# Kernel optimization log

Measured on AMD Instinct MI355X. Metric: run time of the kernel, lower is better.

## Reference

```python
import jax, jax.numpy as jnp
import numpy as np

N_NODES = 100000
N_EDGES = 1600000
D_IN = 128
D_OUT = 128


def setup_inputs() -> dict:
    key = jax.random.key(0)
    k1, k2, k3, k4, k5 = jax.random.split(key, 5)
    features = jax.random.normal(k1, (N_NODES, D_IN), dtype=jnp.float32)
    edge_row = jax.random.randint(k2, (N_EDGES,), 0, N_NODES, dtype=jnp.int32)
    edge_col = jax.random.randint(k3, (N_EDGES,), 0, N_NODES, dtype=jnp.int32)
    edge_val = jax.random.uniform(k4, (N_EDGES,), dtype=jnp.float32)
    # Xavier-uniform weight, zero bias, ones skip weight (matches reset_parameters)
    limit = float(np.sqrt(6.0 / (D_IN + D_OUT)))
    weight = jax.random.uniform(k5, (D_IN, D_OUT), minval=-limit, maxval=limit, dtype=jnp.float32)
    bias = jnp.zeros((D_OUT,), dtype=jnp.float32)
    skip_weight = jnp.ones((D_OUT,), dtype=jnp.float32)
    return {"features": features, "edge_row": edge_row, "edge_col": edge_col,
            "edge_val": edge_val, "weight": weight, "bias": bias,
            "skip_weight": skip_weight}


def reference(features, edge_row, edge_col, edge_val, weight, bias, skip_weight):
    # Dense projection: [N, Din] @ [Din, Dout] -> [N, Dout]
    h = features @ weight
    # SpMM in COO form: Ah[r] = sum_e val[e] * h[col[e]] for edges with row[e]==r
    gathered = edge_val[:, None] * h[edge_col]          # [E, Dout]
    Ah = jax.ops.segment_sum(gathered, edge_row, num_segments=N_NODES)
    # Skip-scale + bias + activation epilogue
    out = h * skip_weight[None, :] + Ah + bias[None, :]
    return jax.nn.selu(out)
```

## Files before the change

### kernel.cpp

```cpp
#include <hip/hip_runtime.h>

#define N_NODES 100000
#define N_EDGES 1600000
#define D 128
#define BM 64
#define GEMM_BLKS 1563

#define BROWS 128
#define NB 782
#define EB 250
#define EPB 6400
#define NTAB (NB * EB)
#define SCAN_BLKS 191

#define SPMM_BLKS 6250

typedef __attribute__((ext_vector_type(8))) short short8_t;
typedef __attribute__((ext_vector_type(4))) float float4_t;
typedef __attribute__((ext_vector_type(2))) float f32x2_t;

__device__ __forceinline__ unsigned pack_bf16x2(float a, float b) {
    unsigned ua = __float_as_uint(a);
    unsigned ub = __float_as_uint(b);
    ua = (ua + 0x7fffu + ((ua >> 16) & 1u)) >> 16;
    ub = (ub + 0x7fffu + ((ub >> 16) & 1u)) & 0xffff0000u;
    return ua | ub;
}

__device__ __forceinline__ float selu_f(float x) {
    const float SCALE = 1.0507009873554805f;
    const float ALPHA = 1.6732632423543772f;
    return x > 0.f ? SCALE * x : SCALE * ALPHA * (expf(x) - 1.f);
}

__global__ __launch_bounds__(256) void bhist_prep_kernel(
    const int* __restrict__ erow, const float* __restrict__ W,
    unsigned* __restrict__ tbl, unsigned short* __restrict__ wt)
{
    __shared__ unsigned hcnt[NB];
    const int t = threadIdx.x;
    if (blockIdx.x < EB) {
        const int k = blockIdx.x;
        for (int i = t; i < NB; i += 256) hcnt[i] = 0;
        __syncthreads();
        const int4* q = (const int4*)(erow + k * EPB);
        for (int i = t; i < EPB / 4; i += 256) {
            const int4 r = q[i];
            atomicAdd(&hcnt[r.x >> 7], 1u);
            atomicAdd(&hcnt[r.y >> 7], 1u);
            atomicAdd(&hcnt[r.z >> 7], 1u);
            atomicAdd(&hcnt[r.w >> 7], 1u);
        }
        __syncthreads();
        for (int i = t; i < NB; i += 256) tbl[k * NB + i] = hcnt[i];
    } else {
        const int pb = blockIdx.x - EB;
        for (int idx = pb * 4096 + t; idx < (pb + 1) * 4096; idx += 256) {
            const int k = idx >> 7, n = idx & 127;
            unsigned u = __float_as_uint(W[idx]);
            u = (u + 0x7fffu + ((u >> 16) & 1u)) >> 16;
            wt[n * D + k] = (unsigned short)u;
        }
    }
}

__global__ __launch_bounds__(1024) void scan_local_kernel(
    const unsigned* __restrict__ tbl, unsigned* __restrict__ lex,
    unsigned* __restrict__ bsum)
{
    __shared__ unsigned wsum[16];
    const int t = threadIdx.x;
    const int L = blockIdx.x * 1024 + t;
    const int lane = t & 63;

    unsigned v = 0;
    if (L < NTAB) {
        const int b = L / EB;
        const int k = L - b * EB;
        v = tbl[k * NB + b];
    }
    unsigned x = v;
#pragma unroll
    for (int d = 1; d < 64; d <<= 1) {
        const unsigned y = __shfl_up(x, d, 64);
        if (lane >= d) x += y;
    }
    if (lane == 63) wsum[t >> 6] = x;
    __syncthreads();
    unsigned add = 0;
    for (int w = 0; w < (t >> 6); ++w) add += wsum[w];
    x += add;
    if (L < NTAB) lex[L] = x - v;
    if (t == 1023) bsum[blockIdx.x] = x;
}

__global__ __launch_bounds__(256) void bscatter_kernel(
    const int* __restrict__ erow, const int* __restrict__ ecol,
    const float* __restrict__ eval_, const unsigned* __restrict__ lex,
    const unsigned* __restrict__ bsum, unsigned* __restrict__ tbl,
    int2* __restrict__ rec)
{
    __shared__ unsigned bp[192];
    __shared__ unsigned wtot[4];
    __shared__ unsigned base[NB], rk[NB];
    const int t = threadIdx.x;
    const int k = blockIdx.x;

    unsigned v = 0, x = 0;
    if (t < 192) {
        v = (t < SCAN_BLKS) ? bsum[t] : 0u;
        x = v;
#pragma unroll
        for (int d = 1; d < 64; d <<= 1) {
            const unsigned y = __shfl_up(x, d, 64);
            if ((t & 63) >= d) x += y;
        }
        if ((t & 63) == 63) wtot[t >> 6] = x;
    }
    __syncthreads();
    if (t < 192) {
        unsigned add = 0;
        if (t >= 64)  add += wtot[0];
        if (t >= 128) add += wtot[1];
        bp[t] = x - v + add;
    }
    __syncthreads();

    for (int b = t; b < NB; b += 256) {
        const int L = b * EB + k;
        const unsigned bs_ = lex[L] + bp[L >> 10];
        base[b] = bs_;
        rk[b] = 0;
        if (k == 0) tbl[b] = bs_;
    }
    __syncthreads();

    const int4*   qr = (const int4*)(erow + k * EPB);
    const int4*   qc = (const int4*)(ecol + k * EPB);
    const float4* qv = (const float4*)(eval_ + k * EPB);

    for (int i = t; i < EPB / 4; i += 256) {
        const int4   r = qr[i];
        const int4   c = qc[i];
        const float4 vv = qv[i];
        {
            const int b = r.x >> 7;
            const unsigned pos = base[b] + atomicAdd(&rk[b], 1u);
            rec[pos] = make_int2(c.x | ((r.x & 127) << 17), __float_as_int(vv.x));
        }
        {
            const int b = r.y >> 7;
            const unsigned pos = base[b] + atomicAdd(&rk[b], 1u);
            rec[pos] = make_int2(c.y | ((r.y & 127) << 17), __float_as_int(vv.y));
        }
        {
            const int b = r.z >> 7;
            const unsigned pos = base[b] + atomicAdd(&rk[b], 1u);
            rec[pos] = make_int2(c.z | ((r.z & 127) << 17), __float_as_int(vv.z));
        }
        {
            const int b = r.w >> 7;
            const unsigned pos = base[b] + atomicAdd(&rk[b], 1u);
            rec[pos] = make_int2(c.w | ((r.w & 127) << 17), __float_as_int(vv.w));
        }
    }
}

__global__ __launch_bounds__(256) void gemm_bsort_kernel(
    const float* __restrict__ feat, const unsigned short* __restrict__ wt,
    unsigned* __restrict__ h16,
    const unsigned* __restrict__ tbl, const int2* __restrict__ rec,
    int2* __restrict__ rec2, unsigned* __restrict__ rstart)
{
    __shared__ __align__(16) char smem[52224];
    const int t = threadIdx.x;

    if (blockIdx.x < GEMM_BLKS) {
        short* At = (short*)smem;
        short* Wt = (short*)(smem + 17408);
        const int rowBase = blockIdx.x * BM;

        {
            const int n = t >> 1, hf = t & 1;
            const uint4* src = (const uint4*)(wt + n * D + hf * 64);
            uint4* dst = (uint4*)&Wt[n * 136 + hf * 64];
#pragma unroll
            for (int j = 0; j < 8; ++j) dst[j] = src[j];
        }
        {
#pragma unroll
            for (int i = 0; i < 8; ++i) {
                const int p = t + 256 * i;
                const int r = p >> 5, kq = p & 31;
                int row = rowBase + r;
                if (row >= N_NODES) row = N_NODES - 1;
                const float4 f = *(const float4*)&feat[(size_t)row * D + kq * 4];
                uint2 u;
                u.x = pack_bf16x2(f.x, f.y);
                u.y = pack_bf16x2(f.z, f.w);
                *(uint2*)&At[r * 136 + kq * 4] = u;
            }
        }
        __syncthreads();

        const int w = t >> 6, lane = t & 63;
        const int m16 = lane & 15, kg = lane >> 4;

        short8_t a_frag[4];
        const int arow = w * 16 + m16;
#pragma unroll
        for (int k0 = 0; k0 < 4; ++k0)
            a_frag[k0] = *(const short8_t*)&At[arow * 136 + k0 * 32 + kg * 8];

#pragma unroll
        for (int nt = 0; nt < 8; ++nt) {
            float4_t acc = {0.f, 0.f, 0.f, 0.f};
#pragma unroll
            for (int k0 = 0; k0 < 4; ++k0) {
                const short8_t b =
                    *(const short8_t*)&Wt[(nt * 16 + m16) * 136 + k0 * 32 + kg * 8];
                acc = __builtin_amdgcn_mfma_f32_16x16x32_bf16(a_frag[k0], b, acc, 0, 0, 0);
            }
            float mine[4], part[4];
#pragma unroll
            for (int i = 0; i < 4; ++i) {
                mine[i] = acc[i];
                part[i] = __shfl_xor(mine[i], 1, 64);
            }
            if ((m16 & 1) == 0) {
                const int cp = (nt * 16 + m16) >> 1;
#pragma unroll
                for (int i = 0; i < 4; ++i) {
                    const int row = rowBase + w * 16 + kg * 4 + i;
                    if (row < N_NODES)
                        h16[(size_t)row * 64 + cp] = pack_bf16x2(mine[i], part[i]);
                }
            }
        }
    } else {
        unsigned* cnt  = (unsigned*)smem;
        unsigned* bas  = cnt + BROWS;
        unsigned* rk   = bas + BROWS;
        unsigned* w0p  = rk + BROWS;
        const int b = blockIdx.x - GEMM_BLKS;

        if (t < BROWS) { cnt[t] = 0; rk[t] = 0; }
        __syncthreads();

        const unsigned s = tbl[b];
        const unsigned e = (b == NB - 1) ? (unsigned)N_EDGES : tbl[b + 1];

        for (unsigned j = s + t; j < e; j += 256)
            atomicAdd(&cnt[(rec[j].x >> 17) & 127], 1u);
        __syncthreads();

        unsigned v = 0, x = 0;
        if (t < BROWS) {
            v = cnt[t]; x = v;
#pragma unroll
            for (int d = 1; d < 64; d <<= 1) {
                const unsigned y = __shfl_up(x, d, 64);
                if ((t & 63) >= d) x += y;
            }
        }
        if (t == 63) w0p[0] = x;
        __syncthreads();
        if (t < BROWS) {
            const unsigned ex = x - v + ((t >= 64) ? w0p[0] : 0u);
            bas[t] = s + ex;
            const int row = b * BROWS + t;
            if (row < N_NODES) rstart[row] = s + ex;
        }
        __syncthreads();

        for (unsigned j = s + t; j < e; j += 256) {
            const int2 R = rec[j];
            const int rl = (R.x >> 17) & 127;
            const unsigned pos = bas[rl] + atomicAdd(&rk[rl], 1u);
            rec2[pos] = R;
        }
    }
}

__global__ __launch_bounds__(256) void spmm_csr_kernel(
    const unsigned* __restrict__ rstart, const int2* __restrict__ rec,
    const unsigned* __restrict__ h16, const float* __restrict__ skip,
    const float* __restrict__ bias, float* __restrict__ out)
{
    const int lane = threadIdx.x & 63;
    const int wid  = threadIdx.x >> 6;
    const int rowBase = (blockIdx.x * 4 + wid) * 4;

    const int c2 = lane * 2;
    const float2 sk = *(const float2*)&skip[c2];
    const float2 bs = *(const float2*)&bias[c2];

    unsigned sb[5];
#pragma unroll
    for (int i = 0; i < 5; ++i) {
        const int rr = rowBase + i;
        const unsigned bnd = (rr < N_NODES) ? rstart[rr] : (unsigned)N_EDGES;
        sb[i] = (unsigned)__builtin_amdgcn_readfirstlane((int)bnd);
    }

#pragma unroll
    for (int r = 0; r < 4; ++r) {
        const int row = rowBase + r;
        const unsigned s = sb[r];
        const unsigned e = sb[r + 1];
        const unsigned n = e - s;
        const unsigned nfull = n >> 3;

        float ax = 0.f, ay = 0.f, bx = 0.f, by = 0.f;

        int2 E0[8], E1[8];
        unsigned g0[8], g1[8];

        auto LOADREC = [&](int2 (&E)[8], unsigned base) {
#pragma unroll
            for (int k = 0; k < 8; ++k) E[k] = rec[base + k];
        };
        auto GATHER = [&](unsigned (&g)[8], const int2 (&E)[8]) {
#pragma unroll
            for (int k = 0; k < 8; ++k)
                g[k] = h16[(size_t)(((unsigned)E[k].x) & 0x1FFFFu) * 64 + lane];
        };
        auto FMA8 = [&](const int2 (&E)[8], const unsigned (&g)[8]) {
#pragma unroll
            for (int k = 0; k < 8; ++k) {
                const float v = __int_as_float(E[k].y);
                if (k & 1) {
                    bx = fmaf(v, __uint_as_float(g[k] << 16), bx);
                    by = fmaf(v, __uint_as_float(g[k] & 0xffff0000u), by);
                } else {
                    ax = fmaf(v, __uint_as_float(g[k] << 16), ax);
                    ay = fmaf(v, __uint_as_float(g[k] & 0xffff0000u), ay);
                }
            }
        };

        if (nfull) {
            LOADREC(E0, s);
            GATHER(g0, E0);
            unsigned bi = 1;
            for (; bi + 1 < nfull; bi += 2) {
                LOADREC(E1, s + bi * 8);
                GATHER(g1, E1);
                FMA8(E0, g0);
                LOADREC(E0, s + (bi + 1) * 8);
                GATHER(g0, E0);
                FMA8(E1, g1);
            }
            if (bi < nfull) {
                LOADREC(E1, s + bi * 8);
                GATHER(g1, E1);
                FMA8(E0, g0);
                FMA8(E1, g1);
            } else {
                FMA8(E0, g0);
            }
        }

        const unsigned tn = n & 7;
        if (tn) {
            const unsigned tb = s + nfull * 8;
            int2 Et[8];
            unsigned gt[8];
#pragma unroll
            for (int k = 0; k < 8; ++k) {
                const unsigned idx = tb + (unsigned)k;
                Et[k] = rec[idx < e ? idx : e - 1u];
            }
#pragma unroll
            for (int k = 0; k < 8; ++k)
                gt[k] = h16[(size_t)(((unsigned)Et[k].x) & 0x1FFFFu) * 64 + lane];
#pragma unroll
            for (int k = 0; k < 8; ++k) {
                const float v = (tb + (unsigned)k < e) ? __int_as_float(Et[k].y) : 0.f;
                if (k & 1) {
                    bx = fmaf(v, __uint_as_float(gt[k] << 16), bx);
                    by = fmaf(v, __uint_as_float(gt[k] & 0xffff0000u), by);
                } else {
                    ax = fmaf(v, __uint_as_float(gt[k] << 16), ax);
                    ay = fmaf(v, __uint_as_float(gt[k] & 0xffff0000u), ay);
                }
            }
        }

        const unsigned hw = h16[(size_t)row * 64 + lane];
        float ox = fmaf(__uint_as_float(hw << 16),         sk.x, (ax + bx) + bs.x);
        float oy = fmaf(__uint_as_float(hw & 0xffff0000u), sk.y, (ay + by) + bs.y);
        ox = selu_f(ox);
        oy = selu_f(oy);
        f32x2_t o;
        o.x = ox;
        o.y = oy;
        __builtin_nontemporal_store(o, (f32x2_t*)&out[(size_t)row * D + c2]);
    }
}

__global__ __launch_bounds__(256) void gemm_fb_kernel(
    const float* __restrict__ feat, const float* __restrict__ W,
    const float* __restrict__ bias, const float* __restrict__ skip,
    float* __restrict__ h, float* __restrict__ out)
{
    __shared__ float Wl[D * D];
    __shared__ float Fl[32 * D];
    const int tid = threadIdx.x;

    const float4* W4 = (const float4*)W;
    float4* Wl4 = (float4*)Wl;
#pragma unroll
    for (int i = 0; i < 16; ++i) Wl4[tid + 256 * i] = W4[tid + 256 * i];

    const size_t rowBase = (size_t)blockIdx.x * 32;
    const float4* F4 = (const float4*)(feat + rowBase * D);
    float4* Fl4 = (float4*)Fl;
#pragma unroll
    for (int i = 0; i < 4; ++i) Fl4[tid + 256 * i] = F4[tid + 256 * i];
    __syncthreads();

    const int colg = (tid & 31) * 4;
    const int row0 = (tid >> 5) * 4;
    float4 acc[4];
#pragma unroll
    for (int r = 0; r < 4; ++r) acc[r] = make_float4(0.f, 0.f, 0.f, 0.f);
#pragma unroll 4
    for (int k = 0; k < D; ++k) {
        const float4 w = *(const float4*)&Wl[k * D + colg];
#pragma unroll
        for (int r = 0; r < 4; ++r) {
            const float aa = Fl[(row0 + r) * D + k];
            acc[r].x += aa * w.x; acc[r].y += aa * w.y;
            acc[r].z += aa * w.z; acc[r].w += aa * w.w;
        }
    }
    const float4 sk = *(const float4*)&skip[colg];
    const float4 bs = *(const float4*)&bias[colg];
#pragma unroll
    for (int r = 0; r < 4; ++r) {
        const size_t row = rowBase + row0 + r;
        *(float4*)&h[row * D + colg] = acc[r];
        float4 o;
        o.x = acc[r].x * sk.x + bs.x; o.y = acc[r].y * sk.y + bs.y;
        o.z = acc[r].z * sk.z + bs.z; o.w = acc[r].w * sk.w + bs.w;
        *(float4*)&out[row * D + colg] = o;
    }
}

__global__ __launch_bounds__(256) void spmm_atomic_kernel(
    const int* __restrict__ erow, const int* __restrict__ ecol,
    const float* __restrict__ eval_, const float* __restrict__ h,
    float* __restrict__ out)
{
    const int e = blockIdx.x * 4 + (threadIdx.x >> 6);
    if (e >= N_EDGES) return;
    const int lane = threadIdx.x & 63;
    const int r = erow[e];
    const int c = ecol[e];
    const float v = eval_[e];
    const float2 hv = *(const float2*)&h[(size_t)c * D + lane * 2];
    float* o = &out[(size_t)r * D + lane * 2];
    atomicAdd(o + 0, v * hv.x);
    atomicAdd(o + 1, v * hv.y);
}

__global__ __launch_bounds__(256) void selu_kernel(float* __restrict__ out)
{
    const size_t i = (size_t)blockIdx.x * blockDim.x + threadIdx.x;
    float4 v = ((float4*)out)[i];
    v.x = selu_f(v.x); v.y = selu_f(v.y); v.z = selu_f(v.z); v.w = selu_f(v.w);
    ((float4*)out)[i] = v;
}

extern "C" void kernel_launch(void* const* d_in, const int* in_sizes, int n_in,
                              void* d_out, int out_size, void* d_ws, size_t ws_size,
                              hipStream_t stream)
{
    const float* feat  = (const float*)d_in[0];
    const int*   erow  = (const int*)d_in[1];
    const int*   ecol  = (const int*)d_in[2];
    const float* eval_ = (const float*)d_in[3];
    const float* W     = (const float*)d_in[4];
    const float* bias  = (const float*)d_in[5];
    const float* skip  = (const float*)d_in[6];

    float* out = (float*)d_out;

    const size_t off_h16  = 0;
    const size_t off_tbl  = 25600000;
    const size_t off_lex  = 26382000;
    const size_t off_bs   = 27164336;
    const size_t off_rst  = 27165360;
    const size_t off_wt   = 27565360;
    const size_t off_rec  = 27598128;
    const size_t off_rec2 = 40398128;
    const size_t needed   = 53198128;

    char* ws = (char*)d_ws;
    unsigned*       h16    = (unsigned*)(ws + off_h16);
    unsigned*       tbl    = (unsigned*)(ws + off_tbl);
    unsigned*       lex    = (unsigned*)(ws + off_lex);
    unsigned*       bsum   = (unsigned*)(ws + off_bs);
    unsigned*       rstart = (unsigned*)(ws + off_rst);
    unsigned short* wt     = (unsigned short*)(ws + off_wt);
    int2*           rec    = (int2*)(ws + off_rec);
    int2*           rec2   = (int2*)(ws + off_rec2);

    if (ws_size >= needed) {
        bhist_prep_kernel<<<EB + 4, 256, 0, stream>>>(erow, W, tbl, wt);
        scan_local_kernel<<<SCAN_BLKS, 1024, 0, stream>>>(tbl, lex, bsum);
        bscatter_kernel<<<EB, 256, 0, stream>>>(erow, ecol, eval_, lex, bsum, tbl, rec);
        gemm_bsort_kernel<<<GEMM_BLKS + NB, 256, 0, stream>>>(
            feat, wt, h16, tbl, rec, rec2, rstart);
        spmm_csr_kernel<<<SPMM_BLKS, 256, 0, stream>>>(
            rstart, rec2, h16, skip, bias, out);
    } else {
        float* h = (float*)d_ws;
        gemm_fb_kernel<<<N_NODES / 32, 256, 0, stream>>>(feat, W, bias, skip, h, out);
        spmm_atomic_kernel<<<N_EDGES / 4, 256, 0, stream>>>(erow, ecol, eval_, h, out);
        selu_kernel<<<(N_NODES * D) / (256 * 4), 256, 0, stream>>>(out);
    }
}
```

Baseline: 125.5 us.

## Split SpMM feature columns across blocks and edges across lane groups

After: 187.4 us. 1.49x slower.

```diff
diff --git a/kernel.cpp b/kernel.cpp
--- a/kernel.cpp
+++ b/kernel.cpp
@@ -13,7 +13,7 @@
 #define NTAB (NB * EB)
 #define SCAN_BLKS 191
 
-#define SPMM_BLKS 6250
+#define SPMM_BLKS 25000
 
 typedef __attribute__((ext_vector_type(8))) short short8_t;
 typedef __attribute__((ext_vector_type(4))) float float4_t;
@@ -289,11 +289,15 @@
 {
     const int lane = threadIdx.x & 63;
     const int wid  = threadIdx.x >> 6;
-    const int rowBase = (blockIdx.x * 4 + wid) * 4;
-
-    const int c2 = lane * 2;
-    const float2 sk = *(const float2*)&skip[c2];
-    const float2 bs = *(const float2*)&bias[c2];
+    const int q    = blockIdx.x & 3;
+    const int rowBase = ((blockIdx.x >> 2) * 4 + wid) * 4;
+
+    const int el  = lane >> 4;
+    const int dwq = (lane & 15) + q * 16;
+    const int c0  = dwq * 2;
+
+    const float skx = skip[c0], sky = skip[c0 + 1];
+    const float bsx = bias[c0], bsy = bias[c0 + 1];
 
     unsigned sb[5];
 #pragma unroll
@@ -308,94 +312,44 @@
         const int row = rowBase + r;
         const unsigned s = sb[r];
         const unsigned e = sb[r + 1];
-        const unsigned n = e - s;
-        const unsigned nfull = n >> 3;
-
-        float ax = 0.f, ay = 0.f, bx = 0.f, by = 0.f;
-
-        int2 E0[8], E1[8];
-        unsigned g0[8], g1[8];
-
-        auto LOADREC = [&](int2 (&E)[8], unsigned base) {
-#pragma unroll
-            for (int k = 0; k < 8; ++k) E[k] = rec[base + k];
-        };
-        auto GATHER = [&](unsigned (&g)[8], const int2 (&E)[8]) {
-#pragma unroll
-            for (int k = 0; k < 8; ++k)
-                g[k] = h16[(size_t)(((unsigned)E[k].x) & 0x1FFFFu) * 64 + lane];
-        };
-        auto FMA8 = [&](const int2 (&E)[8], const unsigned (&g)[8]) {
-#pragma unroll
-            for (int k = 0; k < 8; ++k) {
-                const float v = __int_as_float(E[k].y);
-                if (k & 1) {
-                    bx = fmaf(v, __uint_as_float(g[k] << 16), bx);
-                    by = fmaf(v, __uint_as_float(g[k] & 0xffff0000u), by);
-                } else {
-                    ax = fmaf(v, __uint_as_float(g[k] << 16), ax);
-                    ay = fmaf(v, __uint_as_float(g[k] & 0xffff0000u), ay);
-                }
-            }
-        };
-
-        if (nfull) {
-            LOADREC(E0, s);
-            GATHER(g0, E0);
-            unsigned bi = 1;
-            for (; bi + 1 < nfull; bi += 2) {
-                LOADREC(E1, s + bi * 8);
-                GATHER(g1, E1);
-                FMA8(E0, g0);
-                LOADREC(E0, s + (bi + 1) * 8);
-                GATHER(g0, E0);
-                FMA8(E1, g1);
-            }
-            if (bi < nfull) {
-                LOADREC(E1, s + bi * 8);
-                GATHER(g1, E1);
-                FMA8(E0, g0);
-                FMA8(E1, g1);
-            } else {
-                FMA8(E0, g0);
-            }
-        }
-
-        const unsigned tn = n & 7;
-        if (tn) {
-            const unsigned tb = s + nfull * 8;
-            int2 Et[8];
-            unsigned gt[8];
-#pragma unroll
-            for (int k = 0; k < 8; ++k) {
-                const unsigned idx = tb + (unsigned)k;
-                Et[k] = rec[idx < e ? idx : e - 1u];
-            }
-#pragma unroll
-            for (int k = 0; k < 8; ++k)
-                gt[k] = h16[(size_t)(((unsigned)Et[k].x) & 0x1FFFFu) * 64 + lane];
-#pragma unroll
-            for (int k = 0; k < 8; ++k) {
-                const float v = (tb + (unsigned)k < e) ? __int_as_float(Et[k].y) : 0.f;
-                if (k & 1) {
-                    bx = fmaf(v, __uint_as_float(gt[k] << 16), bx);
-                    by = fmaf(v, __uint_as_float(gt[k] & 0xffff0000u), by);
-                } else {
-                    ax = fmaf(v, __uint_as_float(gt[k] << 16), ax);
-                    ay = fmaf(v, __uint_as_float(gt[k] & 0xffff0000u), ay);
-                }
-            }
-        }
-
-        const unsigned hw = h16[(size_t)row * 64 + lane];
-        float ox = fmaf(__uint_as_float(hw << 16),         sk.x, (ax + bx) + bs.x);
-        float oy = fmaf(__uint_as_float(hw & 0xffff0000u), sk.y, (ay + by) + bs.y);
-        ox = selu_f(ox);
-        oy = selu_f(oy);
-        f32x2_t o;
-        o.x = ox;
-        o.y = oy;
-        __builtin_nontemporal_store(o, (f32x2_t*)&out[(size_t)row * D + c2]);
+
+        float ax = 0.f, ay = 0.f;
+
+        for (unsigned j = s; j < e; j += 16) {
+            int2     E[4];
+            unsigned g[4];
+            float    v[4];
+#pragma unroll
+            for (int k = 0; k < 4; ++k) {
+                const unsigned idx = j + (unsigned)(el + 4 * k);
+                const unsigned ji  = idx < e ? idx : e - 1u;
+                E[k] = rec[ji];
+                v[k] = (idx < e) ? __int_as_float(E[k].y) : 0.f;
+            }
+#pragma unroll
+            for (int k = 0; k < 4; ++k)
+                g[k] = h16[(size_t)(((unsigned)E[k].x) & 0x1FFFFu) * 64 + dwq];
+#pragma unroll
+            for (int k = 0; k < 4; ++k) {
+                ax = fmaf(v[k], __uint_as_float(g[k] << 16), ax);
+                ay = fmaf(v[k], __uint_as_float(g[k] & 0xffff0000u), ay);
+            }
+        }
+
+        ax += __shfl_xor(ax, 16, 64);
+        ax += __shfl_xor(ax, 32, 64);
+        ay += __shfl_xor(ay, 16, 64);
+        ay += __shfl_xor(ay, 32, 64);
+
+        if (el == 0) {
+            const unsigned hw = h16[(size_t)row * 64 + dwq];
+            float ox = fmaf(__uint_as_float(hw << 16),         skx, ax + bsx);
+            float oy = fmaf(__uint_as_float(hw & 0xffff0000u), sky, ay + bsy);
+            f32x2_t o;
+            o.x = selu_f(ox);
+            o.y = selu_f(oy);
+            __builtin_nontemporal_store(o, (f32x2_t*)&out[(size_t)row * D + c0]);
+        }
     }
 }
 
```
